# Optimization experiments

Measured on AMD Instinct MI355X. Metric: run time of the kernel, lower is better.

Reference implementation:

```python
import jax, jax.numpy as jnp
import numpy as np

EPS = 1e-5
NUM_HEAD = 8
D_MODEL = 512
D_K = D_MODEL // NUM_HEAD
SCALE = np.float32(1.0 / np.sqrt(D_K))


def _ln(x, g, b):
    m = jnp.mean(x, axis=-1, keepdims=True)
    v = jnp.var(x, axis=-1, keepdims=True)
    return g * (x - m) * jax.lax.rsqrt(v + EPS) + b


def setup_inputs() -> dict:
    key = jax.random.key(0)
    ks = jax.random.split(key, 24)
    B, W, S, V, D = 16, 256, 16, 32, D_MODEL
    DF = 2 * D
    w = lambda k, shape: (jax.random.normal(k, shape, jnp.float32) * 0.02)
    inp = {
        "text": jax.random.normal(ks[0], (B, W, D), jnp.float32),
        "av_feat": jax.random.normal(ks[1], (B, S, V, D), jnp.float32),
        "text_mask": jnp.ones((B, W, W), dtype=bool),
        "attn_sent_index": jnp.sort(jax.random.randint(ks[2], (B, W), 0, S), axis=-1),
        # res1 LayerNorm
        "ln_res1_g": jnp.ones((D,), jnp.float32), "ln_res1_b": jnp.zeros((D,), jnp.float32),
        # self-attention projections
        "sa_wq": w(ks[3], (D, D)), "sa_bq": jnp.zeros((D,), jnp.float32),
        "sa_wk": w(ks[4], (D, D)), "sa_bk": jnp.zeros((D,), jnp.float32),
        "sa_wv": w(ks[5], (D, D)), "sa_bv": jnp.zeros((D,), jnp.float32),
        "sa_wo": w(ks[6], (D, D)), "sa_bo": jnp.zeros((D,), jnp.float32),
        # cross-attention norms + projections
        "ca_ln_text_g": jnp.ones((D,), jnp.float32), "ca_ln_text_b": jnp.zeros((D,), jnp.float32),
        "ca_ln_av_g": jnp.ones((D,), jnp.float32), "ca_ln_av_b": jnp.zeros((D,), jnp.float32),
        "ca_wq": w(ks[7], (D, D)), "ca_bq": jnp.zeros((D,), jnp.float32),
        "ca_wk": w(ks[8], (D, D)), "ca_bk": jnp.zeros((D,), jnp.float32),
        "ca_wv": w(ks[9], (D, D)), "ca_bv": jnp.zeros((D,), jnp.float32),
        # post-cross norms
        "ln1_g": jnp.ones((D,), jnp.float32), "ln1_b": jnp.zeros((D,), jnp.float32),
        "ln2_g": jnp.ones((D,), jnp.float32), "ln2_b": jnp.zeros((D,), jnp.float32),
        # res2 LayerNorm + FFN (d_ff = 2*d_model per source)
        "ln_res2_g": jnp.ones((D,), jnp.float32), "ln_res2_b": jnp.zeros((D,), jnp.float32),
        "ff_w1": w(ks[10], (D, DF)), "ff_b1": jnp.zeros((DF,), jnp.float32),
        "ff_w2": w(ks[11], (DF, D)), "ff_b2": jnp.zeros((D,), jnp.float32),
    }
    return inp


def reference(text, av_feat, text_mask, attn_sent_index,
              ln_res1_g, ln_res1_b,
              sa_wq, sa_bq, sa_wk, sa_bk, sa_wv, sa_bv, sa_wo, sa_bo,
              ca_ln_text_g, ca_ln_text_b, ca_ln_av_g, ca_ln_av_b,
              ca_wq, ca_bq, ca_wk, ca_bk, ca_wv, ca_bv,
              ln1_g, ln1_b, ln2_g, ln2_b,
              ln_res2_g, ln_res2_b, ff_w1, ff_b1, ff_w2, ff_b2):
    B, W, D = text.shape
    S, V = av_feat.shape[1], av_feat.shape[2]

    # ---- res1: x + self_attn(norm(x)) (dropout = identity in eval) ----
    x = _ln(text, ln_res1_g, ln_res1_b)
    q = (x @ sa_wq + sa_bq).reshape(B, W, NUM_HEAD, D_K)
    k = (x @ sa_wk + sa_bk).reshape(B, W, NUM_HEAD, D_K)
    v = (x @ sa_wv + sa_bv).reshape(B, W, NUM_HEAD, D_K)
    scores = jnp.einsum('bqhd,bkhd->bhqk', q, k) * SCALE
    scores = jnp.where(text_mask[:, None, :, :], scores, jnp.float32(-1e9))
    a = jax.nn.softmax(scores, axis=-1)
    sa = jnp.einsum('bhqk,bkhd->bqhd', a, v).reshape(B, W, D) @ sa_wo + sa_bo
    text = text + sa

    # ---- cross attention: index-gathered sigmoid attention ----
    tn = _ln(text, ca_ln_text_g, ca_ln_text_b)
    an = _ln(av_feat, ca_ln_av_g, ca_ln_av_b)
    cq = (tn @ ca_wq + ca_bq).reshape(B, W, 1, NUM_HEAD, D_K)
    ck = (an @ ca_wk + ca_bk).reshape(B, S, V, NUM_HEAD, D_K)
    cv = (an @ ca_wv + ca_bv).reshape(B, S, V, NUM_HEAD, D_K)
    bidx = jnp.arange(B)[:, None]
    ck = ck[bidx, attn_sent_index]  # [B, W, V, H, Dk]
    cv = cv[bidx, attn_sent_index]  # [B, W, V, H, Dk]
    att = jax.nn.sigmoid(jnp.sum(cq * ck, axis=-1, keepdims=True) * SCALE)  # [B,W,V,H,1]
    res = jnp.sum(att * cv, axis=-3).reshape(B, W, D)

    text = _ln(text, ln1_g, ln1_b) + _ln(res, ln2_g, ln2_b)  # av_weight = 1

    # ---- res2: x + FFN(norm(x)) ----
    y = _ln(text, ln_res2_g, ln_res2_b)
    text = text + (jax.nn.relu(y @ ff_w1 + ff_b1) @ ff_w2 + ff_b2)

    attn_out = jnp.mean(att, axis=-2)[..., 0]  # mean over heads -> [B, W, V]
    return (text, attn_out)
```

## Files before the change

kernel.cpp:

```cpp
#include <hip/hip_runtime.h>
#include <hip/hip_bf16.h>


#define D_MODEL 512
#define NUM_HEAD 8
#define D_K 64
#define SCALE 0.125f
#define EPS 1e-5f

typedef __hip_bfloat16 bf16;
typedef __attribute__((ext_vector_type(8))) short short8;
typedef __attribute__((ext_vector_type(4))) float floatx4;

static __device__ __forceinline__ float bf2f(bf16 x) { return __bfloat162float(x); }
static __device__ __forceinline__ float s2f(short u) {
    unsigned int x = ((unsigned int)(unsigned short)u) << 16;
    float f; __builtin_memcpy(&f, &x, 4); return f;
}
static __device__ __forceinline__ short f2s(float f) {
    bf16 t = __float2bfloat16(f);
    short s; __builtin_memcpy(&s, &t, 2); return s;
}

struct TransArgs {
    const float* src[9];
    bf16* dst[9];
    int K[9], N[9];
    int start[10];
};

__global__ __launch_bounds__(256) void transpose_kernel(TransArgs a) {
    int bid = blockIdx.x;
    int m = 0;
    while (bid >= a.start[m + 1]) m++;
    const int t = bid - a.start[m];
    const int N = a.N[m], K = a.K[m];
    const int tilesX = N >> 5;
    const int tx = t % tilesX, ty = t / tilesX;
    __shared__ bf16 tile[32][33];
    const int tid = threadIdx.x;
    const int r = tid >> 3, c0 = (tid & 7) * 4;
    const float* sp = a.src[m] + (size_t)(ty * 32 + r) * N + tx * 32 + c0;
    float4 v = *(const float4*)sp;
    tile[r][c0 + 0] = __float2bfloat16(v.x);
    tile[r][c0 + 1] = __float2bfloat16(v.y);
    tile[r][c0 + 2] = __float2bfloat16(v.z);
    tile[r][c0 + 3] = __float2bfloat16(v.w);
    __syncthreads();
    bf16* dp = a.dst[m] + (size_t)(tx * 32 + r) * K + ty * 32 + c0;
    #pragma unroll
    for (int i = 0; i < 4; i++) dp[i] = tile[c0 + i][r];
}

__global__ __launch_bounds__(256) void ln_kernel(const float* __restrict__ inp,
                                                 const float* __restrict__ g,
                                                 const float* __restrict__ bta,
                                                 bf16* __restrict__ out) {
    const size_t row = blockIdx.x;
    const int t = threadIdx.x;
    const float x0 = inp[row * D_MODEL + t];
    const float x1 = inp[row * D_MODEL + t + 256];
    float s = x0 + x1, sq = x0 * x0 + x1 * x1;
    #pragma unroll
    for (int off = 32; off >= 1; off >>= 1) {
        s += __shfl_xor(s, off, 64);
        sq += __shfl_xor(sq, off, 64);
    }
    __shared__ float ws_[4], wq_[4];
    if ((t & 63) == 0) { ws_[t >> 6] = s; wq_[t >> 6] = sq; }
    __syncthreads();
    s = ws_[0] + ws_[1] + ws_[2] + ws_[3];
    sq = wq_[0] + wq_[1] + wq_[2] + wq_[3];
    const float m = s * (1.f / D_MODEL);
    const float var = sq * (1.f / D_MODEL) - m * m;
    const float r = rsqrtf(var + EPS);
    out[row * D_MODEL + t]       = __float2bfloat16(g[t]       * (x0 - m) * r + bta[t]);
    out[row * D_MODEL + t + 256] = __float2bfloat16(g[t + 256] * (x1 - m) * r + bta[t + 256]);
}

__global__ __launch_bounds__(256) void ln2_add_ln_kernel(const float* __restrict__ a,
                                                         const float* __restrict__ c,
                                                         const float* __restrict__ g1,
                                                         const float* __restrict__ b1,
                                                         const float* __restrict__ g2,
                                                         const float* __restrict__ b2,
                                                         const float* __restrict__ g3,
                                                         const float* __restrict__ b3,
                                                         float* __restrict__ text2,
                                                         bf16* __restrict__ y) {
    const size_t row = blockIdx.x;
    const int t = threadIdx.x;
    const float a0 = a[row * D_MODEL + t], a1 = a[row * D_MODEL + t + 256];
    const float c0 = c[row * D_MODEL + t], c1 = c[row * D_MODEL + t + 256];
    float sa = a0 + a1, qa = a0 * a0 + a1 * a1;
    float sc = c0 + c1, qc = c0 * c0 + c1 * c1;
    #pragma unroll
    for (int off = 32; off >= 1; off >>= 1) {
        sa += __shfl_xor(sa, off, 64); qa += __shfl_xor(qa, off, 64);
        sc += __shfl_xor(sc, off, 64); qc += __shfl_xor(qc, off, 64);
    }
    __shared__ float r_[4][4];
    if ((t & 63) == 0) { int w = t >> 6; r_[0][w] = sa; r_[1][w] = qa; r_[2][w] = sc; r_[3][w] = qc; }
    __syncthreads();
    sa = r_[0][0] + r_[0][1] + r_[0][2] + r_[0][3];
    qa = r_[1][0] + r_[1][1] + r_[1][2] + r_[1][3];
    sc = r_[2][0] + r_[2][1] + r_[2][2] + r_[2][3];
    qc = r_[3][0] + r_[3][1] + r_[3][2] + r_[3][3];
    const float ma = sa * (1.f / D_MODEL), mc = sc * (1.f / D_MODEL);
    const float ra = rsqrtf(qa * (1.f / D_MODEL) - ma * ma + EPS);
    const float rc = rsqrtf(qc * (1.f / D_MODEL) - mc * mc + EPS);
    const float v0 = g1[t] * (a0 - ma) * ra + b1[t] + g2[t] * (c0 - mc) * rc + b2[t];
    const float v1 = g1[t + 256] * (a1 - ma) * ra + b1[t + 256]
                   + g2[t + 256] * (c1 - mc) * rc + b2[t + 256];
    text2[row * D_MODEL + t] = v0;
    text2[row * D_MODEL + t + 256] = v1;
    float sv = v0 + v1, qv = v0 * v0 + v1 * v1;
    #pragma unroll
    for (int off = 32; off >= 1; off >>= 1) {
        sv += __shfl_xor(sv, off, 64); qv += __shfl_xor(qv, off, 64);
    }
    __syncthreads();
    if ((t & 63) == 0) { int w = t >> 6; r_[0][w] = sv; r_[1][w] = qv; }
    __syncthreads();
    sv = r_[0][0] + r_[0][1] + r_[0][2] + r_[0][3];
    qv = r_[1][0] + r_[1][1] + r_[1][2] + r_[1][3];
    const float mv = sv * (1.f / D_MODEL);
    const float rv = rsqrtf(qv * (1.f / D_MODEL) - mv * mv + EPS);
    y[row * D_MODEL + t]       = __float2bfloat16(g3[t]       * (v0 - mv) * rv + b3[t]);
    y[row * D_MODEL + t + 256] = __float2bfloat16(g3[t + 256] * (v1 - mv) * rv + b3[t + 256]);
}

template <int RES, bool RELU, bool OUT_BF16>
__global__ __launch_bounds__(256) void gemm2(const bf16* __restrict__ A,
                                             const bf16* __restrict__ BT,
                                             const float* __restrict__ bias,
                                             const float* __restrict__ resid,
                                             void* __restrict__ C,
                                             int M, int N, int K) {
    __shared__ short As[128 * 72];
    __shared__ short Bs[64 * 72];
    const int tid = threadIdx.x;
    const int lane = tid & 63, w = tid >> 6;
    const int quad = lane >> 4, l15 = lane & 15;
    const int wm = (w >> 1) * 64, wn = (w & 1) * 32;
    const int m0 = blockIdx.y * 128, n0 = blockIdx.x * 64;
    const short* Ag = (const short*)A;
    const short* Bg = (const short*)BT;
    floatx4 acc[4][2] = {};
    for (int kk0 = 0; kk0 < K; kk0 += 64) {
        #pragma unroll
        for (int p = 0; p < 4; p++) {
            const int e = p * 2048 + tid * 8;
            const int row = e >> 6, col = e & 63;
            *(short8*)&As[row * 72 + col] = *(const short8*)&Ag[(size_t)(m0 + row) * K + kk0 + col];
        }
        #pragma unroll
        for (int p = 0; p < 2; p++) {
            const int e = p * 2048 + tid * 8;
            const int row = e >> 6, col = e & 63;
            *(short8*)&Bs[row * 72 + col] = *(const short8*)&Bg[(size_t)(n0 + row) * K + kk0 + col];
        }
        __syncthreads();
        #pragma unroll
        for (int ks = 0; ks < 2; ks++) {
            const int kc = ks * 32 + quad * 8;
            short8 b0 = *(const short8*)&Bs[(wn + l15) * 72 + kc];
            short8 b1 = *(const short8*)&Bs[(wn + 16 + l15) * 72 + kc];
            #pragma unroll
            for (int mi = 0; mi < 4; mi++) {
                short8 am = *(const short8*)&As[(wm + mi * 16 + l15) * 72 + kc];
                acc[mi][0] = __builtin_amdgcn_mfma_f32_16x16x32_bf16(am, b0, acc[mi][0], 0, 0, 0);
                acc[mi][1] = __builtin_amdgcn_mfma_f32_16x16x32_bf16(am, b1, acc[mi][1], 0, 0, 0);
            }
        }
        __syncthreads();
    }
    #pragma unroll
    for (int mi = 0; mi < 4; mi++)
        #pragma unroll
        for (int ni = 0; ni < 2; ni++)
            #pragma unroll
            for (int r = 0; r < 4; r++) {
                const int row = m0 + wm + mi * 16 + quad * 4 + r;
                const int col = n0 + wn + ni * 16 + l15;
                float v = acc[mi][ni][r] + bias[col];
                if (RELU) v = fmaxf(v, 0.f);
                if (RES == 1) v += resid[(size_t)row * N + col];
                if (OUT_BF16) ((bf16*)C)[(size_t)row * N + col] = __float2bfloat16(v);
                else          ((float*)C)[(size_t)row * N + col] = v;
            }
}

__global__ __launch_bounds__(256) void gemm_fused(const bf16* __restrict__ A,
                                                  const bf16* __restrict__ BT,
                                                  const float* __restrict__ b0p,
                                                  const float* __restrict__ b1p,
                                                  const float* __restrict__ b2p,
                                                  bf16* __restrict__ C,
                                                  int M, int Ntot, int K) {
    __shared__ short As[128 * 72];
    __shared__ short Bs[64 * 72];
    const int tid = threadIdx.x;
    const int lane = tid & 63, w = tid >> 6;
    const int quad = lane >> 4, l15 = lane & 15;
    const int wm = (w >> 1) * 64, wn = (w & 1) * 32;
    const int m0 = blockIdx.y * 128, n0 = blockIdx.x * 64;
    const int seg = n0 >> 9;
    const float* bias = (seg == 0) ? b0p : ((seg == 1) ? b1p : b2p);
    const short* Ag = (const short*)A;
    const short* Bg = (const short*)BT;
    floatx4 acc[4][2] = {};
    for (int kk0 = 0; kk0 < K; kk0 += 64) {
        #pragma unroll
        for (int p = 0; p < 4; p++) {
            const int e = p * 2048 + tid * 8;
            const int row = e >> 6, col = e & 63;
            *(short8*)&As[row * 72 + col] = *(const short8*)&Ag[(size_t)(m0 + row) * K + kk0 + col];
        }
        #pragma unroll
        for (int p = 0; p < 2; p++) {
            const int e = p * 2048 + tid * 8;
            const int row = e >> 6, col = e & 63;
            *(short8*)&Bs[row * 72 + col] = *(const short8*)&Bg[(size_t)(n0 + row) * K + kk0 + col];
        }
        __syncthreads();
        #pragma unroll
        for (int ks = 0; ks < 2; ks++) {
            const int kc = ks * 32 + quad * 8;
            short8 b0 = *(const short8*)&Bs[(wn + l15) * 72 + kc];
            short8 b1 = *(const short8*)&Bs[(wn + 16 + l15) * 72 + kc];
            #pragma unroll
            for (int mi = 0; mi < 4; mi++) {
                short8 am = *(const short8*)&As[(wm + mi * 16 + l15) * 72 + kc];
                acc[mi][0] = __builtin_amdgcn_mfma_f32_16x16x32_bf16(am, b0, acc[mi][0], 0, 0, 0);
                acc[mi][1] = __builtin_amdgcn_mfma_f32_16x16x32_bf16(am, b1, acc[mi][1], 0, 0, 0);
            }
        }
        __syncthreads();
    }
    #pragma unroll
    for (int mi = 0; mi < 4; mi++)
        #pragma unroll
        for (int ni = 0; ni < 2; ni++)
            #pragma unroll
            for (int r = 0; r < 4; r++) {
                const int row = m0 + wm + mi * 16 + quad * 4 + r;
                const int col = n0 + wn + ni * 16 + l15;
                C[(size_t)row * Ntot + col] = __float2bfloat16(acc[mi][ni][r] + bias[col & 511]);
            }
}

__global__ __launch_bounds__(256) void self_attn_mfma(const bf16* __restrict__ q,
                                                      const bf16* __restrict__ k,
                                                      const bf16* __restrict__ v,
                                                      int ld,
                                                      bf16* __restrict__ sa) {
    const int qc = blockIdx.x, h = blockIdx.y, b = blockIdx.z;
    const int tid = threadIdx.x, lane = tid & 63, w = tid >> 6;
    const int quad = lane >> 4, l15 = lane & 15;
    __shared__ short Kt[64 * 72];
    __shared__ short VT[64 * 72];
    __shared__ short Ps[4][16 * 72];
    const int qrow = b * 256 + qc * 64 + w * 16 + l15;
    const short* qg = (const short*)q + (size_t)qrow * ld + h * 64;
    short8 qf0 = *(const short8*)&qg[quad * 8];
    short8 qf1 = *(const short8*)&qg[32 + quad * 8];
    floatx4 o[4] = {};
    float den[4] = {};
    for (int kt0 = 0; kt0 < 256; kt0 += 64) {
        __syncthreads();
        {
            const int row = tid >> 2, c0 = (tid & 3) * 16;
            const short* kg = (const short*)k + (size_t)(b * 256 + kt0 + row) * ld + h * 64 + c0;
            *(short8*)&Kt[row * 72 + c0]     = *(const short8*)kg;
            *(short8*)&Kt[row * 72 + c0 + 8] = *(const short8*)(kg + 8);
        }
        {
            const int key = tid & 63, dk0 = (tid >> 6) * 16;
            const short* vg = (const short*)v + (size_t)(b * 256 + kt0 + key) * ld + h * 64 + dk0;
            short8 v0 = *(const short8*)vg;
            short8 v1 = *(const short8*)(vg + 8);
            #pragma unroll
            for (int i = 0; i < 8; i++) VT[(dk0 + i) * 72 + key] = v0[i];
            #pragma unroll
            for (int i = 0; i < 8; i++) VT[(dk0 + 8 + i) * 72 + key] = v1[i];
        }
        __syncthreads();
        floatx4 sacc[4] = {};
        #pragma unroll
        for (int ni = 0; ni < 4; ni++) {
            short8 b0 = *(const short8*)&Kt[(ni * 16 + l15) * 72 + quad * 8];
            short8 b1 = *(const short8*)&Kt[(ni * 16 + l15) * 72 + 32 + quad * 8];
            sacc[ni] = __builtin_amdgcn_mfma_f32_16x16x32_bf16(qf0, b0, sacc[ni], 0, 0, 0);
            sacc[ni] = __builtin_amdgcn_mfma_f32_16x16x32_bf16(qf1, b1, sacc[ni], 0, 0, 0);
        }
        #pragma unroll
        for (int ni = 0; ni < 4; ni++)
            #pragma unroll
            for (int r = 0; r < 4; r++) {
                const float e = __expf(sacc[ni][r] * SCALE);
                den[r] += e;
                Ps[w][(quad * 4 + r) * 72 + ni * 16 + l15] = f2s(e);
            }
        #pragma unroll
        for (int kc = 0; kc < 2; kc++) {
            short8 af = *(const short8*)&Ps[w][l15 * 72 + kc * 32 + quad * 8];
            #pragma unroll
            for (int ni = 0; ni < 4; ni++) {
                short8 bv = *(const short8*)&VT[(ni * 16 + l15) * 72 + kc * 32 + quad * 8];
                o[ni] = __builtin_amdgcn_mfma_f32_16x16x32_bf16(af, bv, o[ni], 0, 0, 0);
            }
        }
    }
    #pragma unroll
    for (int off = 1; off < 16; off <<= 1)
        #pragma unroll
        for (int r = 0; r < 4; r++) den[r] += __shfl_xor(den[r], off, 64);
    float inv[4];
    #pragma unroll
    for (int r = 0; r < 4; r++) inv[r] = 1.f / den[r];
    const int qo = b * 256 + qc * 64 + w * 16 + quad * 4;
    #pragma unroll
    for (int ni = 0; ni < 4; ni++)
        #pragma unroll
        for (int r = 0; r < 4; r++)
            sa[(size_t)(qo + r) * D_MODEL + h * 64 + ni * 16 + l15] =
                __float2bfloat16(o[ni][r] * inv[r]);
}

__global__ __launch_bounds__(256) void cross_attn3(const bf16* __restrict__ kv,
                                                   const float* __restrict__ cq,
                                                   const int* __restrict__ sidx,
                                                   float* __restrict__ res,
                                                   float* __restrict__ out_attn) {
    const int s = blockIdx.x, b = blockIdx.y, t = threadIdx.x;
    __shared__ int wrange[2];
    __shared__ short Ks[32 * 576];
    __shared__ short Vs[32 * 576];
    __shared__ short qs[32 * 576];
    __shared__ float att[32 * 256];
    if (t == 0) { wrange[0] = 256; wrange[1] = 0; }
    __syncthreads();
    const int* sb = sidx + b * 256;
    {
        const int sv = sb[t];
        if (sv == s) {
            if (t == 0 || sb[t - 1] != s) wrange[0] = t;
            if (t == 255 || sb[t + 1] != s) wrange[1] = t + 1;
        }
    }
    {
        const int v = t >> 3, hh = t & 7;
        const short* kg = (const short*)kv + ((size_t)((b * 16 + s) * 32 + v)) * 1024 + hh * 64;
        const short* vg = kg + 512;
        short* kd = &Ks[v * 576 + hh * 72];
        short* vd = &Vs[v * 576 + hh * 72];
        #pragma unroll
        for (int c = 0; c < 8; c++) {
            *(short8*)&kd[c * 8] = *(const short8*)&kg[c * 8];
            *(short8*)&vd[c * 8] = *(const short8*)&vg[c * 8];
        }
    }
    __syncthreads();
    const int w0 = wrange[0], w1 = wrange[1];
    const int h2 = t >> 5, dp = t & 31;
    for (int wc = w0; wc < w1; wc += 32) {
        const int len = (w1 - wc < 32) ? (w1 - wc) : 32;
        for (int i = t; i < len * 256; i += 256) {
            const int f = i * 2;
            const int row = f >> 9, col = f & 511;
            float2 q2 = *(const float2*)&cq[((size_t)(b * 256 + wc + row)) * 512 + col];
            short* qd = &qs[row * 576 + (col >> 6) * 72 + (col & 63)];
            qd[0] = f2s(q2.x);
            qd[1] = f2s(q2.y);
        }
        __syncthreads();
        for (int i = t; i < len * 256; i += 256) {
            const int wl = i >> 8, r = i & 255, v = r >> 3, h = r & 7;
            const short* qp = &qs[wl * 576 + h * 72];
            const short* kp = &Ks[v * 576 + h * 72];
            float dot = 0.f;
            #pragma unroll
            for (int c = 0; c < 8; c++) {
                short8 q8 = *(const short8*)&qp[c * 8];
                short8 k8 = *(const short8*)&kp[c * 8];
                dot += s2f(q8[0]) * s2f(k8[0]) + s2f(q8[1]) * s2f(k8[1])
                     + s2f(q8[2]) * s2f(k8[2]) + s2f(q8[3]) * s2f(k8[3])
                     + s2f(q8[4]) * s2f(k8[4]) + s2f(q8[5]) * s2f(k8[5])
                     + s2f(q8[6]) * s2f(k8[6]) + s2f(q8[7]) * s2f(k8[7]);
            }
            att[wl * 256 + r] = 1.f / (1.f + __expf(-dot * SCALE));
        }
        __syncthreads();
        for (int wl = 0; wl < len; wl++) {
            float r0 = 0.f, r1 = 0.f;
            #pragma unroll
            for (int vv = 0; vv < 32; ++vv) {
                const float av = att[wl * 256 + vv * 8 + h2];
                const int pv = *(const int*)&Vs[vv * 576 + h2 * 72 + dp * 2];
                r0 += av * s2f((short)(pv & 0xffff));
                r1 += av * s2f((short)(pv >> 16));
            }
            *(float2*)&res[((size_t)(b * 256 + wc + wl)) * 512 + h2 * 64 + dp * 2] =
                make_float2(r0, r1);
        }
        if (t < 32) {
            for (int wl = 0; wl < len; wl++) {
                float m = 0.f;
                #pragma unroll
                for (int j = 0; j < 8; j++) m += att[wl * 256 + t * 8 + j];
                out_attn[((size_t)(b * 256 + wc + wl)) * 32 + t] = m * 0.125f;
            }
        }
        __syncthreads();
    }
}

extern "C" void kernel_launch(void* const* d_in, const int* in_sizes, int n_in,
                              void* d_out, int out_size, void* d_ws, size_t ws_size,
                              hipStream_t stream) {
    const int B = 16, S = 16;
    const int M1 = 4096, M2 = 8192;

    const float* text = (const float*)d_in[0];
    const float* av   = (const float*)d_in[1];
    const int* sidx   = (const int*)d_in[3];
    const float* ln_res1_g = (const float*)d_in[4];
    const float* ln_res1_b = (const float*)d_in[5];
    const float* sa_wq = (const float*)d_in[6];
    const float* sa_bq = (const float*)d_in[7];
    const float* sa_wk = (const float*)d_in[8];
    const float* sa_bk = (const float*)d_in[9];
    const float* sa_wv = (const float*)d_in[10];
    const float* sa_bv = (const float*)d_in[11];
    const float* sa_wo = (const float*)d_in[12];
    const float* sa_bo = (const float*)d_in[13];
    const float* ca_ln_text_g = (const float*)d_in[14];
    const float* ca_ln_text_b = (const float*)d_in[15];
    const float* ca_ln_av_g = (const float*)d_in[16];
    const float* ca_ln_av_b = (const float*)d_in[17];
    const float* ca_wq = (const float*)d_in[18];
    const float* ca_bq = (const float*)d_in[19];
    const float* ca_wk = (const float*)d_in[20];
    const float* ca_bk = (const float*)d_in[21];
    const float* ca_wv = (const float*)d_in[22];
    const float* ca_bv = (const float*)d_in[23];
    const float* ln1_g = (const float*)d_in[24];
    const float* ln1_b = (const float*)d_in[25];
    const float* ln2_g = (const float*)d_in[26];
    const float* ln2_b = (const float*)d_in[27];
    const float* ln_res2_g = (const float*)d_in[28];
    const float* ln_res2_b = (const float*)d_in[29];
    const float* ff_w1 = (const float*)d_in[30];
    const float* ff_b1 = (const float*)d_in[31];
    const float* ff_w2 = (const float*)d_in[32];
    const float* ff_b2 = (const float*)d_in[33];

    char* wsb = (char*)d_ws;
    const size_t MBy = 1024 * 1024;
    bf16*  WT    = (bf16*)(wsb);
    float* text1 = (float*)(wsb + 6 * MBy);
    bf16*  xln   = (bf16*)(wsb + 14 * MBy);
    bf16*  qkv   = (bf16*)(wsb + 18 * MBy);
    bf16*  sab   = (bf16*)(wsb + 30 * MBy);
    bf16*  tn    = (bf16*)(wsb + 14 * MBy);
    bf16*  an    = (bf16*)(wsb + 34 * MBy);
    float* cq    = (float*)(wsb + 42 * MBy);
    bf16*  kvb   = (bf16*)(wsb + 50 * MBy);
    float* res   = (float*)(wsb + 18 * MBy);
    float* text2 = (float*)(wsb + 26 * MBy);
    bf16*  y     = (bf16*)(wsb + 34 * MBy);
    bf16*  h1    = (bf16*)(wsb + 42 * MBy);

    bf16* wqT  = WT;
    bf16* cwqT = WT + 1048576;
    bf16* cwkT = WT + 1310720;
    bf16* woT  = WT + 786432;
    bf16* f1T  = WT + 1835008;
    bf16* f2T  = WT + 2359296;

    float* out_text = (float*)d_out;
    float* out_attn = (float*)d_out + (size_t)M1 * D_MODEL;

    TransArgs ta;
    const float* srcs[9] = {sa_wq, sa_wk, sa_wv, sa_wo, ca_wq, ca_wk, ca_wv, ff_w1, ff_w2};
    bf16* dsts[9] = {wqT, WT + 262144, WT + 524288, woT, cwqT, cwkT, WT + 1572864, f1T, f2T};
    const int Ks_[9] = {512, 512, 512, 512, 512, 512, 512, 512, 1024};
    const int Ns_[9] = {512, 512, 512, 512, 512, 512, 512, 1024, 512};
    int cum = 0;
    for (int i = 0; i < 9; i++) {
        ta.src[i] = srcs[i]; ta.dst[i] = dsts[i]; ta.K[i] = Ks_[i]; ta.N[i] = Ns_[i];
        ta.start[i] = cum;
        cum += (Ks_[i] >> 5) * (Ns_[i] >> 5);
    }
    ta.start[9] = cum;
    transpose_kernel<<<cum, 256, 0, stream>>>(ta);

    const dim3 blk256(256);
    const dim3 gD(D_MODEL / 64, M1 / 128);
    const dim3 gQKV(1536 / 64, M1 / 128);
    const dim3 gKV(1024 / 64, M2 / 128);
    const dim3 gF1(1024 / 64, M1 / 128);

    ln_kernel<<<M1, blk256, 0, stream>>>(text, ln_res1_g, ln_res1_b, xln);
    gemm_fused<<<gQKV, blk256, 0, stream>>>(xln, wqT, sa_bq, sa_bk, sa_bv, qkv, M1, 1536, D_MODEL);
    self_attn_mfma<<<dim3(4, NUM_HEAD, B), blk256, 0, stream>>>(qkv, qkv + 512, qkv + 1024, 1536, sab);
    gemm2<1, false, false><<<gD, blk256, 0, stream>>>(sab, woT, sa_bo, text, text1, M1, D_MODEL, D_MODEL);
    ln_kernel<<<M1, blk256, 0, stream>>>(text1, ca_ln_text_g, ca_ln_text_b, tn);
    ln_kernel<<<M2, blk256, 0, stream>>>(av, ca_ln_av_g, ca_ln_av_b, an);
    gemm2<0, false, false><<<gD, blk256, 0, stream>>>(tn, cwqT, ca_bq, nullptr, cq, M1, D_MODEL, D_MODEL);
    gemm_fused<<<gKV, blk256, 0, stream>>>(an, cwkT, ca_bk, ca_bv, ca_bv, kvb, M2, 1024, D_MODEL);
    cross_attn3<<<dim3(S, B), blk256, 0, stream>>>(kvb, cq, sidx, res, out_attn);
    ln2_add_ln_kernel<<<M1, blk256, 0, stream>>>(text1, res, ln1_g, ln1_b, ln2_g, ln2_b,
                                                 ln_res2_g, ln_res2_b, text2, y);
    gemm2<0, true, true><<<gF1, blk256, 0, stream>>>(y, f1T, ff_b1, nullptr, h1, M1, 1024, D_MODEL);
    gemm2<1, false, false><<<gD, blk256, 0, stream>>>(h1, f2T, ff_b2, text2, out_text, M1, D_MODEL, 1024);
}
```

Before: 287.6 us.

## Fuse LayerNorms into GEMM prologues and merge cross-attn projection launches

Removes the standalone LayerNorm kernels. Each GEMM now computes per-row mean and rstd and normalises its fp32 A tile on the fly before the bf16 MFMA. The cross-attention Q and K/V projections are merged into one launch, and the cq buffer is now bf16. The FF1 GEMM recomputes the ln1+ln2+res2 chain per tile and writes text2 only from the n0==0 blocks. This cuts launches and intermediate bf16 round-trips, but every N-tile re-reads the fp32 A rows and repeats the normalisation work.

```diff
diff --git a/kernel.cpp b/kernel.cpp
--- a/kernel.cpp
+++ b/kernel.cpp
@@ -4,7 +4,6 @@
 
 #define D_MODEL 512
 #define NUM_HEAD 8
-#define D_K 64
 #define SCALE 0.125f
 #define EPS 1e-5f
 
@@ -12,7 +11,6 @@
 typedef __attribute__((ext_vector_type(8))) short short8;
 typedef __attribute__((ext_vector_type(4))) float floatx4;
 
-static __device__ __forceinline__ float bf2f(bf16 x) { return __bfloat162float(x); }
 static __device__ __forceinline__ float s2f(short u) {
     unsigned int x = ((unsigned int)(unsigned short)u) << 16;
     float f; __builtin_memcpy(&f, &x, 4); return f;
@@ -50,84 +48,6 @@
     bf16* dp = a.dst[m] + (size_t)(tx * 32 + r) * K + ty * 32 + c0;
     #pragma unroll
     for (int i = 0; i < 4; i++) dp[i] = tile[c0 + i][r];
-}
-
-__global__ __launch_bounds__(256) void ln_kernel(const float* __restrict__ inp,
-                                                 const float* __restrict__ g,
-                                                 const float* __restrict__ bta,
-                                                 bf16* __restrict__ out) {
-    const size_t row = blockIdx.x;
-    const int t = threadIdx.x;
-    const float x0 = inp[row * D_MODEL + t];
-    const float x1 = inp[row * D_MODEL + t + 256];
-    float s = x0 + x1, sq = x0 * x0 + x1 * x1;
-    #pragma unroll
-    for (int off = 32; off >= 1; off >>= 1) {
-        s += __shfl_xor(s, off, 64);
-        sq += __shfl_xor(sq, off, 64);
-    }
-    __shared__ float ws_[4], wq_[4];
-    if ((t & 63) == 0) { ws_[t >> 6] = s; wq_[t >> 6] = sq; }
-    __syncthreads();
-    s = ws_[0] + ws_[1] + ws_[2] + ws_[3];
-    sq = wq_[0] + wq_[1] + wq_[2] + wq_[3];
-    const float m = s * (1.f / D_MODEL);
-    const float var = sq * (1.f / D_MODEL) - m * m;
-    const float r = rsqrtf(var + EPS);
-    out[row * D_MODEL + t]       = __float2bfloat16(g[t]       * (x0 - m) * r + bta[t]);
-    out[row * D_MODEL + t + 256] = __float2bfloat16(g[t + 256] * (x1 - m) * r + bta[t + 256]);
-}
-
-__global__ __launch_bounds__(256) void ln2_add_ln_kernel(const float* __restrict__ a,
-                                                         const float* __restrict__ c,
-                                                         const float* __restrict__ g1,
-                                                         const float* __restrict__ b1,
-                                                         const float* __restrict__ g2,
-                                                         const float* __restrict__ b2,
-                                                         const float* __restrict__ g3,
-                                                         const float* __restrict__ b3,
-                                                         float* __restrict__ text2,
-                                                         bf16* __restrict__ y) {
-    const size_t row = blockIdx.x;
-    const int t = threadIdx.x;
-    const float a0 = a[row * D_MODEL + t], a1 = a[row * D_MODEL + t + 256];
-    const float c0 = c[row * D_MODEL + t], c1 = c[row * D_MODEL + t + 256];
-    float sa = a0 + a1, qa = a0 * a0 + a1 * a1;
-    float sc = c0 + c1, qc = c0 * c0 + c1 * c1;
-    #pragma unroll
-    for (int off = 32; off >= 1; off >>= 1) {
-        sa += __shfl_xor(sa, off, 64); qa += __shfl_xor(qa, off, 64);
-        sc += __shfl_xor(sc, off, 64); qc += __shfl_xor(qc, off, 64);
-    }
-    __shared__ float r_[4][4];
-    if ((t & 63) == 0) { int w = t >> 6; r_[0][w] = sa; r_[1][w] = qa; r_[2][w] = sc; r_[3][w] = qc; }
-    __syncthreads();
-    sa = r_[0][0] + r_[0][1] + r_[0][2] + r_[0][3];
-    qa = r_[1][0] + r_[1][1] + r_[1][2] + r_[1][3];
-    sc = r_[2][0] + r_[2][1] + r_[2][2] + r_[2][3];
-    qc = r_[3][0] + r_[3][1] + r_[3][2] + r_[3][3];
-    const float ma = sa * (1.f / D_MODEL), mc = sc * (1.f / D_MODEL);
-    const float ra = rsqrtf(qa * (1.f / D_MODEL) - ma * ma + EPS);
-    const float rc = rsqrtf(qc * (1.f / D_MODEL) - mc * mc + EPS);
-    const float v0 = g1[t] * (a0 - ma) * ra + b1[t] + g2[t] * (c0 - mc) * rc + b2[t];
-    const float v1 = g1[t + 256] * (a1 - ma) * ra + b1[t + 256]
-                   + g2[t + 256] * (c1 - mc) * rc + b2[t + 256];
-    text2[row * D_MODEL + t] = v0;
-    text2[row * D_MODEL + t + 256] = v1;
-    float sv = v0 + v1, qv = v0 * v0 + v1 * v1;
-    #pragma unroll
-    for (int off = 32; off >= 1; off >>= 1) {
-        sv += __shfl_xor(sv, off, 64); qv += __shfl_xor(qv, off, 64);
-    }
-    __syncthreads();
-    if ((t & 63) == 0) { int w = t >> 6; r_[0][w] = sv; r_[1][w] = qv; }
-    __syncthreads();
-    sv = r_[0][0] + r_[0][1] + r_[0][2] + r_[0][3];
-    qv = r_[1][0] + r_[1][1] + r_[1][2] + r_[1][3];
-    const float mv = sv * (1.f / D_MODEL);
-    const float rv = rsqrtf(qv * (1.f / D_MODEL) - mv * mv + EPS);
-    y[row * D_MODEL + t]       = __float2bfloat16(g3[t]       * (v0 - mv) * rv + b3[t]);
-    y[row * D_MODEL + t + 256] = __float2bfloat16(g3[t + 256] * (v1 - mv) * rv + b3[t + 256]);
 }
 
 template <int RES, bool RELU, bool OUT_BF16>
@@ -191,49 +111,256 @@
             }
 }
 
-__global__ __launch_bounds__(256) void gemm_fused(const bf16* __restrict__ A,
-                                                  const bf16* __restrict__ BT,
-                                                  const float* __restrict__ b0p,
-                                                  const float* __restrict__ b1p,
-                                                  const float* __restrict__ b2p,
-                                                  bf16* __restrict__ C,
-                                                  int M, int Ntot, int K) {
+static __device__ __forceinline__ void gemm_ln_body(
+    const float* __restrict__ A, const bf16* __restrict__ BT,
+    const float* __restrict__ bA, const float* __restrict__ bB, const float* __restrict__ bC,
+    bf16* __restrict__ C, int N, int m0, int n0,
+    const float* __restrict__ lng, const float* __restrict__ lnb,
+    short* As, short* Bs, float* m_, float* r_, float* lngs, float* lnbs,
+    float* sred, float* qred)
+{
+    const int tid = threadIdx.x;
+    const int lane = tid & 63, w = tid >> 6;
+    const int quad = lane >> 4, l15 = lane & 15;
+    const int wm = (w >> 1) * 64, wn = (w & 1) * 32;
+    for (int i = tid; i < 512; i += 256) { lngs[i] = lng[i]; lnbs[i] = lnb[i]; }
+    {
+        const float* p = A + (size_t)(m0 + (tid >> 1)) * 512 + (tid & 1) * 256;
+        float s = 0.f, q = 0.f;
+        #pragma unroll 8
+        for (int c = 0; c < 256; c += 4) {
+            float4 v = *(const float4*)&p[c];
+            s += v.x + v.y + v.z + v.w;
+            q += v.x * v.x + v.y * v.y + v.z * v.z + v.w * v.w;
+        }
+        sred[tid] = s; qred[tid] = q;
+    }
+    __syncthreads();
+    if (tid < 128) {
+        const float s = sred[2 * tid] + sred[2 * tid + 1];
+        const float q = qred[2 * tid] + qred[2 * tid + 1];
+        const float m = s * (1.f / 512.f);
+        m_[tid] = m;
+        r_[tid] = rsqrtf(q * (1.f / 512.f) - m * m + EPS);
+    }
+    __syncthreads();
+    const short* Bg = (const short*)BT;
+    floatx4 acc[4][2] = {};
+    for (int kk0 = 0; kk0 < 512; kk0 += 64) {
+        #pragma unroll
+        for (int p = 0; p < 4; p++) {
+            const int e = p * 2048 + tid * 8;
+            const int row = e >> 6, col = e & 63;
+            const int gcol = kk0 + col;
+            const float* ap = A + (size_t)(m0 + row) * 512 + gcol;
+            float4 x0 = *(const float4*)ap;
+            float4 x1 = *(const float4*)(ap + 4);
+            const float mm = m_[row], rr = r_[row];
+            short8 vv;
+            vv[0] = f2s((x0.x - mm) * rr * lngs[gcol + 0] + lnbs[gcol + 0]);
+            vv[1] = f2s((x0.y - mm) * rr * lngs[gcol + 1] + lnbs[gcol + 1]);
+            vv[2] = f2s((x0.z - mm) * rr * lngs[gcol + 2] + lnbs[gcol + 2]);
+            vv[3] = f2s((x0.w - mm) * rr * lngs[gcol + 3] + lnbs[gcol + 3]);
+            vv[4] = f2s((x1.x - mm) * rr * lngs[gcol + 4] + lnbs[gcol + 4]);
+            vv[5] = f2s((x1.y - mm) * rr * lngs[gcol + 5] + lnbs[gcol + 5]);
+            vv[6] = f2s((x1.z - mm) * rr * lngs[gcol + 6] + lnbs[gcol + 6]);
+            vv[7] = f2s((x1.w - mm) * rr * lngs[gcol + 7] + lnbs[gcol + 7]);
+            *(short8*)&As[row * 72 + col] = vv;
+        }
+        #pragma unroll
+        for (int p = 0; p < 2; p++) {
+            const int e = p * 2048 + tid * 8;
+            const int row = e >> 6, col = e & 63;
+            *(short8*)&Bs[row * 72 + col] = *(const short8*)&Bg[(size_t)(n0 + row) * 512 + kk0 + col];
+        }
+        __syncthreads();
+        #pragma unroll
+        for (int ks = 0; ks < 2; ks++) {
+            const int kc = ks * 32 + quad * 8;
+            short8 b0 = *(const short8*)&Bs[(wn + l15) * 72 + kc];
+            short8 b1 = *(const short8*)&Bs[(wn + 16 + l15) * 72 + kc];
+            #pragma unroll
+            for (int mi = 0; mi < 4; mi++) {
+                short8 am = *(const short8*)&As[(wm + mi * 16 + l15) * 72 + kc];
+                acc[mi][0] = __builtin_amdgcn_mfma_f32_16x16x32_bf16(am, b0, acc[mi][0], 0, 0, 0);
+                acc[mi][1] = __builtin_amdgcn_mfma_f32_16x16x32_bf16(am, b1, acc[mi][1], 0, 0, 0);
+            }
+        }
+        __syncthreads();
+    }
+    const int seg = n0 >> 9;
+    const float* bias = (seg == 0) ? bA : ((seg == 1) ? bB : bC);
+    #pragma unroll
+    for (int mi = 0; mi < 4; mi++)
+        #pragma unroll
+        for (int ni = 0; ni < 2; ni++)
+            #pragma unroll
+            for (int r = 0; r < 4; r++) {
+                const int row = m0 + wm + mi * 16 + quad * 4 + r;
+                const int col = n0 + wn + ni * 16 + l15;
+                C[(size_t)row * N + col] = __float2bfloat16(acc[mi][ni][r] + bias[col & 511]);
+            }
+}
+
+__global__ __launch_bounds__(256) void gemm_ln_qkv(const float* __restrict__ A,
+                                                   const bf16* __restrict__ BT,
+                                                   const float* __restrict__ lng,
+                                                   const float* __restrict__ lnb,
+                                                   const float* __restrict__ bA,
+                                                   const float* __restrict__ bB,
+                                                   const float* __restrict__ bC,
+                                                   bf16* __restrict__ C) {
     __shared__ short As[128 * 72];
     __shared__ short Bs[64 * 72];
+    __shared__ float m_[128], r_[128], lngs[512], lnbs[512], sred[256], qred[256];
+    gemm_ln_body(A, BT, bA, bB, bC, C, 1536, blockIdx.y * 128, blockIdx.x * 64,
+                 lng, lnb, As, Bs, m_, r_, lngs, lnbs, sred, qred);
+}
+
+__global__ __launch_bounds__(256) void gemm_ln_dual(
+    const float* __restrict__ A1, const bf16* __restrict__ BT1,
+    const float* __restrict__ lng1, const float* __restrict__ lnb1,
+    const float* __restrict__ bias1, bf16* __restrict__ C1,
+    const float* __restrict__ A2, const bf16* __restrict__ BT2,
+    const float* __restrict__ lng2, const float* __restrict__ lnb2,
+    const float* __restrict__ b2a, const float* __restrict__ b2b,
+    bf16* __restrict__ C2) {
+    __shared__ short As[128 * 72];
+    __shared__ short Bs[64 * 72];
+    __shared__ float m_[128], r_[128], lngs[512], lnbs[512], sred[256], qred[256];
+    const int bid = blockIdx.x;
+    if (bid < 256) {
+        gemm_ln_body(A1, BT1, bias1, bias1, bias1, C1, 512, (bid >> 3) * 128, (bid & 7) * 64,
+                     lng1, lnb1, As, Bs, m_, r_, lngs, lnbs, sred, qred);
+    } else {
+        const int r = bid - 256;
+        gemm_ln_body(A2, BT2, b2a, b2b, b2b, C2, 1024, (r >> 4) * 128, (r & 15) * 64,
+                     lng2, lnb2, As, Bs, m_, r_, lngs, lnbs, sred, qred);
+    }
+}
+
+__global__ __launch_bounds__(256) void gemm_ff1(const float* __restrict__ a,
+                                                const float* __restrict__ c,
+                                                const float* __restrict__ g1, const float* __restrict__ b1,
+                                                const float* __restrict__ g2, const float* __restrict__ b2,
+                                                const float* __restrict__ g3, const float* __restrict__ b3,
+                                                const bf16* __restrict__ BT,
+                                                const float* __restrict__ bias,
+                                                float* __restrict__ text2,
+                                                bf16* __restrict__ C) {
+    __shared__ short As[128 * 72];
+    __shared__ short Bs[64 * 72];
+    __shared__ float ma_[128], ra_[128], mc_[128], rc_[128], mv_[128], rv_[128];
+    __shared__ float g1s[512], b1s[512], g2s[512], b2s[512], g3s[512], b3s[512];
+    __shared__ float s1[256], q1[256], s2[256], q2[256];
     const int tid = threadIdx.x;
     const int lane = tid & 63, w = tid >> 6;
     const int quad = lane >> 4, l15 = lane & 15;
     const int wm = (w >> 1) * 64, wn = (w & 1) * 32;
     const int m0 = blockIdx.y * 128, n0 = blockIdx.x * 64;
-    const int seg = n0 >> 9;
-    const float* bias = (seg == 0) ? b0p : ((seg == 1) ? b1p : b2p);
-    const short* Ag = (const short*)A;
+    for (int i = tid; i < 512; i += 256) {
+        g1s[i] = g1[i]; b1s[i] = b1[i];
+        g2s[i] = g2[i]; b2s[i] = b2[i];
+        g3s[i] = g3[i]; b3s[i] = b3[i];
+    }
+    {
+        const float* pa = a + (size_t)(m0 + (tid >> 1)) * 512 + (tid & 1) * 256;
+        const float* pc = c + (size_t)(m0 + (tid >> 1)) * 512 + (tid & 1) * 256;
+        float sa = 0.f, qa = 0.f, sc = 0.f, qc = 0.f;
+        #pragma unroll 8
+        for (int i2 = 0; i2 < 256; i2 += 4) {
+            float4 va = *(const float4*)&pa[i2];
+            float4 vc = *(const float4*)&pc[i2];
+            sa += va.x + va.y + va.z + va.w;
+            qa += va.x * va.x + va.y * va.y + va.z * va.z + va.w * va.w;
+            sc += vc.x + vc.y + vc.z + vc.w;
+            qc += vc.x * vc.x + vc.y * vc.y + vc.z * vc.z + vc.w * vc.w;
+        }
+        s1[tid] = sa; q1[tid] = qa; s2[tid] = sc; q2[tid] = qc;
+    }
+    __syncthreads();
+    if (tid < 128) {
+        float s = s1[2 * tid] + s1[2 * tid + 1], q = q1[2 * tid] + q1[2 * tid + 1];
+        float m = s * (1.f / 512.f);
+        ma_[tid] = m; ra_[tid] = rsqrtf(q * (1.f / 512.f) - m * m + EPS);
+        s = s2[2 * tid] + s2[2 * tid + 1]; q = q2[2 * tid] + q2[2 * tid + 1];
+        m = s * (1.f / 512.f);
+        mc_[tid] = m; rc_[tid] = rsqrtf(q * (1.f / 512.f) - m * m + EPS);
+    }
+    __syncthreads();
+    {
+        const int lr = tid >> 1;
+        const int row = m0 + lr, off = (tid & 1) * 256;
+        const float* pa = a + (size_t)row * 512 + off;
+        const float* pc = c + (size_t)row * 512 + off;
+        const float maa = ma_[lr], raa = ra_[lr], mcc = mc_[lr], rcc = rc_[lr];
+        float sv = 0.f, qv = 0.f;
+        #pragma unroll 8
+        for (int i2 = 0; i2 < 256; i2 += 4) {
+            float4 va = *(const float4*)&pa[i2];
+            float4 vc = *(const float4*)&pc[i2];
+            const int g = off + i2;
+            float4 t;
+            t.x = g1s[g + 0] * (va.x - maa) * raa + b1s[g + 0] + g2s[g + 0] * (vc.x - mcc) * rcc + b2s[g + 0];
+            t.y = g1s[g + 1] * (va.y - maa) * raa + b1s[g + 1] + g2s[g + 1] * (vc.y - mcc) * rcc + b2s[g + 1];
+            t.z = g1s[g + 2] * (va.z - maa) * raa + b1s[g + 2] + g2s[g + 2] * (vc.z - mcc) * rcc + b2s[g + 2];
+            t.w = g1s[g + 3] * (va.w - maa) * raa + b1s[g + 3] + g2s[g + 3] * (vc.w - mcc) * rcc + b2s[g + 3];
+            sv += t.x + t.y + t.z + t.w;
+            qv += t.x * t.x + t.y * t.y + t.z * t.z + t.w * t.w;
+            if (n0 == 0) *(float4*)&text2[(size_t)row * 512 + g] = t;
+        }
+        s1[tid] = sv; q1[tid] = qv;
+    }
+    __syncthreads();
+    if (tid < 128) {
+        const float s = s1[2 * tid] + s1[2 * tid + 1], q = q1[2 * tid] + q1[2 * tid + 1];
+        const float m = s * (1.f / 512.f);
+        mv_[tid] = m; rv_[tid] = rsqrtf(q * (1.f / 512.f) - m * m + EPS);
+    }
+    __syncthreads();
     const short* Bg = (const short*)BT;
     floatx4 acc[4][2] = {};
-    for (int kk0 = 0; kk0 < K; kk0 += 64) {
+    for (int kk0 = 0; kk0 < 512; kk0 += 64) {
         #pragma unroll
         for (int p = 0; p < 4; p++) {
             const int e = p * 2048 + tid * 8;
             const int row = e >> 6, col = e & 63;
-            *(short8*)&As[row * 72 + col] = *(const short8*)&Ag[(size_t)(m0 + row) * K + kk0 + col];
+            const int gcol = kk0 + col;
+            const float* pa = a + (size_t)(m0 + row) * 512 + gcol;
+            const float* pc = c + (size_t)(m0 + row) * 512 + gcol;
+            float4 a0 = *(const float4*)pa, a1 = *(const float4*)(pa + 4);
+            float4 c0 = *(const float4*)pc, c1 = *(const float4*)(pc + 4);
+            const float maa = ma_[row], raa = ra_[row], mcc = mc_[row], rcc = rc_[row];
+            const float mvv = mv_[row], rvv = rv_[row];
+            float av[8] = {a0.x, a0.y, a0.z, a0.w, a1.x, a1.y, a1.z, a1.w};
+            float cv[8] = {c0.x, c0.y, c0.z, c0.w, c1.x, c1.y, c1.z, c1.w};
+            short8 vv;
+            #pragma unroll
+            for (int i = 0; i < 8; i++) {
+                const int g = gcol + i;
+                const float t = g1s[g] * (av[i] - maa) * raa + b1s[g]
+                              + g2s[g] * (cv[i] - mcc) * rcc + b2s[g];
+                vv[i] = f2s(g3s[g] * (t - mvv) * rvv + b3s[g]);
+            }
+            *(short8*)&As[row * 72 + col] = vv;
         }
         #pragma unroll
         for (int p = 0; p < 2; p++) {
             const int e = p * 2048 + tid * 8;
             const int row = e >> 6, col = e & 63;
-            *(short8*)&Bs[row * 72 + col] = *(const short8*)&Bg[(size_t)(n0 + row) * K + kk0 + col];
+            *(short8*)&Bs[row * 72 + col] = *(const short8*)&Bg[(size_t)(n0 + row) * 512 + kk0 + col];
         }
         __syncthreads();
         #pragma unroll
         for (int ks = 0; ks < 2; ks++) {
             const int kc = ks * 32 + quad * 8;
-            short8 b0 = *(const short8*)&Bs[(wn + l15) * 72 + kc];
-            short8 b1 = *(const short8*)&Bs[(wn + 16 + l15) * 72 + kc];
+            short8 b0f = *(const short8*)&Bs[(wn + l15) * 72 + kc];
+            short8 b1f = *(const short8*)&Bs[(wn + 16 + l15) * 72 + kc];
             #pragma unroll
             for (int mi = 0; mi < 4; mi++) {
                 short8 am = *(const short8*)&As[(wm + mi * 16 + l15) * 72 + kc];
-                acc[mi][0] = __builtin_amdgcn_mfma_f32_16x16x32_bf16(am, b0, acc[mi][0], 0, 0, 0);
-                acc[mi][1] = __builtin_amdgcn_mfma_f32_16x16x32_bf16(am, b1, acc[mi][1], 0, 0, 0);
+                acc[mi][0] = __builtin_amdgcn_mfma_f32_16x16x32_bf16(am, b0f, acc[mi][0], 0, 0, 0);
+                acc[mi][1] = __builtin_amdgcn_mfma_f32_16x16x32_bf16(am, b1f, acc[mi][1], 0, 0, 0);
             }
         }
         __syncthreads();
@@ -246,7 +373,8 @@
             for (int r = 0; r < 4; r++) {
                 const int row = m0 + wm + mi * 16 + quad * 4 + r;
                 const int col = n0 + wn + ni * 16 + l15;
-                C[(size_t)row * Ntot + col] = __float2bfloat16(acc[mi][ni][r] + bias[col & 511]);
+                const float v = fmaxf(acc[mi][ni][r] + bias[col], 0.f);
+                C[(size_t)row * 1024 + col] = __float2bfloat16(v);
             }
 }
 
@@ -329,7 +457,7 @@
 }
 
 __global__ __launch_bounds__(256) void cross_attn3(const bf16* __restrict__ kv,
-                                                   const float* __restrict__ cq,
+                                                   const bf16* __restrict__ cq,
                                                    const int* __restrict__ sidx,
                                                    float* __restrict__ res,
                                                    float* __restrict__ out_attn) {
@@ -364,15 +492,14 @@
     __syncthreads();
     const int w0 = wrange[0], w1 = wrange[1];
     const int h2 = t >> 5, dp = t & 31;
+    const short* cqg = (const short*)cq;
     for (int wc = w0; wc < w1; wc += 32) {
         const int len = (w1 - wc < 32) ? (w1 - wc) : 32;
-        for (int i = t; i < len * 256; i += 256) {
-            const int f = i * 2;
-            const int row = f >> 9, col = f & 511;
-            float2 q2 = *(const float2*)&cq[((size_t)(b * 256 + wc + row)) * 512 + col];
-            short* qd = &qs[row * 576 + (col >> 6) * 72 + (col & 63)];
-            qd[0] = f2s(q2.x);
-            qd[1] = f2s(q2.y);
+        for (int i = t; i < len * 64; i += 256) {
+            const int e = i * 8;
+            const int row = e >> 9, col = e & 511;
+            *(short8*)&qs[row * 576 + (col >> 6) * 72 + (col & 63)] =
+                *(const short8*)&cqg[((size_t)(b * 256 + wc + row)) * 512 + col];
         }
         __syncthreads();
         for (int i = t; i < len * 256; i += 256) {
@@ -460,17 +587,13 @@
     const size_t MBy = 1024 * 1024;
     bf16*  WT    = (bf16*)(wsb);
     float* text1 = (float*)(wsb + 6 * MBy);
-    bf16*  xln   = (bf16*)(wsb + 14 * MBy);
-    bf16*  qkv   = (bf16*)(wsb + 18 * MBy);
-    bf16*  sab   = (bf16*)(wsb + 30 * MBy);
-    bf16*  tn    = (bf16*)(wsb + 14 * MBy);
-    bf16*  an    = (bf16*)(wsb + 34 * MBy);
-    float* cq    = (float*)(wsb + 42 * MBy);
-    bf16*  kvb   = (bf16*)(wsb + 50 * MBy);
-    float* res   = (float*)(wsb + 18 * MBy);
-    float* text2 = (float*)(wsb + 26 * MBy);
-    bf16*  y     = (bf16*)(wsb + 34 * MBy);
-    bf16*  h1    = (bf16*)(wsb + 42 * MBy);
+    bf16*  qkv   = (bf16*)(wsb + 14 * MBy);
+    bf16*  sab   = (bf16*)(wsb + 26 * MBy);
+    bf16*  kvb   = (bf16*)(wsb + 30 * MBy);
+    bf16*  cqb   = (bf16*)(wsb + 46 * MBy);
+    float* res   = (float*)(wsb + 50 * MBy);
+    float* text2 = (float*)(wsb + 58 * MBy);
+    bf16*  h1    = (bf16*)(wsb + 66 * MBy);
 
     bf16* wqT  = WT;
     bf16* cwqT = WT + 1048576;
@@ -497,22 +620,17 @@
     transpose_kernel<<<cum, 256, 0, stream>>>(ta);
 
     const dim3 blk256(256);
-    const dim3 gD(D_MODEL / 64, M1 / 128);
-    const dim3 gQKV(1536 / 64, M1 / 128);
-    const dim3 gKV(1024 / 64, M2 / 128);
-    const dim3 gF1(1024 / 64, M1 / 128);
-
-    ln_kernel<<<M1, blk256, 0, stream>>>(text, ln_res1_g, ln_res1_b, xln);
-    gemm_fused<<<gQKV, blk256, 0, stream>>>(xln, wqT, sa_bq, sa_bk, sa_bv, qkv, M1, 1536, D_MODEL);
+
+    gemm_ln_qkv<<<dim3(24, 32), blk256, 0, stream>>>(text, wqT, ln_res1_g, ln_res1_b,
+                                                     sa_bq, sa_bk, sa_bv, qkv);
     self_attn_mfma<<<dim3(4, NUM_HEAD, B), blk256, 0, stream>>>(qkv, qkv + 512, qkv + 1024, 1536, sab);
-    gemm2<1, false, false><<<gD, blk256, 0, stream>>>(sab, woT, sa_bo, text, text1, M1, D_MODEL, D_MODEL);
-    ln_kernel<<<M1, blk256, 0, stream>>>(text1, ca_ln_text_g, ca_ln_text_b, tn);
-    ln_kernel<<<M2, blk256, 0, stream>>>(av, ca_ln_av_g, ca_ln_av_b, an);
-    gemm2<0, false, false><<<gD, blk256, 0, stream>>>(tn, cwqT, ca_bq, nullptr, cq, M1, D_MODEL, D_MODEL);
-    gemm_fused<<<gKV, blk256, 0, stream>>>(an, cwkT, ca_bk, ca_bv, ca_bv, kvb, M2, 1024, D_MODEL);
-    cross_attn3<<<dim3(S, B), blk256, 0, stream>>>(kvb, cq, sidx, res, out_attn);
-    ln2_add_ln_kernel<<<M1, blk256, 0, stream>>>(text1, res, ln1_g, ln1_b, ln2_g, ln2_b,
-                                                 ln_res2_g, ln_res2_b, text2, y);
-    gemm2<0, true, true><<<gF1, blk256, 0, stream>>>(y, f1T, ff_b1, nullptr, h1, M1, 1024, D_MODEL);
-    gemm2<1, false, false><<<gD, blk256, 0, stream>>>(h1, f2T, ff_b2, text2, out_text, M1, D_MODEL, 1024);
-}
+    gemm2<1, false, false><<<dim3(8, 32), blk256, 0, stream>>>(sab, woT, sa_bo, text, text1,
+                                                               M1, D_MODEL, D_MODEL);
+    gemm_ln_dual<<<1280, blk256, 0, stream>>>(text1, cwqT, ca_ln_text_g, ca_ln_text_b, ca_bq, cqb,
+                                              av, cwkT, ca_ln_av_g, ca_ln_av_b, ca_bk, ca_bv, kvb);
+    cross_attn3<<<dim3(S, B), blk256, 0, stream>>>(kvb, cqb, sidx, res, out_attn);
+    gemm_ff1<<<dim3(16, 32), blk256, 0, stream>>>(text1, res, ln1_g, ln1_b, ln2_g, ln2_b,
+                                                  ln_res2_g, ln_res2_b, f1T, ff_b1, text2, h1);
+    gemm2<1, false, false><<<dim3(8, 32), blk256, 0, stream>>>(h1, f2T, ff_b2, text2, out_text,
+                                                               M1, D_MODEL, 1024);
+}
```

New measurement: 497.0 us. 72.8% more time.
